# Performance work log

Hardware: AMD Instinct MI355X
Metric: run time of the kernel (lower is better)

Reference implementation:

```python
import jax, jax.numpy as jnp
import numpy as np

B, N, DM, H = 1, 2048, 1024, 16
CURV = 1.0  # hyperbolic curvature


def setup_inputs() -> dict:
    key = jax.random.key(0)
    ks = jax.random.split(key, 5)
    s = 1.0 / np.sqrt(DM)  # nn.Linear default init scale
    x = jax.random.normal(ks[0], (B, N, DM), dtype=jnp.float32)
    Wq = jax.random.uniform(ks[1], (DM, DM), jnp.float32, -s, s)
    Wk = jax.random.uniform(ks[2], (DM, DM), jnp.float32, -s, s)
    Wv = jax.random.uniform(ks[3], (DM, DM), jnp.float32, -s, s)
    Wo = jax.random.uniform(ks[4], (DM, DM), jnp.float32, -s, s)
    return {"x": x, "Wq": Wq, "Wk": Wk, "Wv": Wv, "Wo": Wo}


def reference(x, Wq, Wk, Wv, Wo):
    b, n, d = x.shape
    hd = d // H

    def split_heads(t):  # [B,N,D] -> [B,H,N,hd]
        return t.reshape(b, n, H, hd).transpose(0, 2, 1, 3)

    q = split_heads(x @ Wq.T)
    k = split_heads(x @ Wk.T)
    v = split_heads(x @ Wv.T)

    q_norm_sq = jnp.sum(q * q, axis=-1, keepdims=True)      # [B,H,N,1]
    k_norm_sq = jnp.sum(k * k, axis=-1)[:, :, None, :]      # [B,H,1,N]
    qk = jnp.einsum('bhnd,bhmd->bhnm', q, k)                # [B,H,N,N]

    diff_sq = jnp.maximum(q_norm_sq + k_norm_sq - 2.0 * qk, 0.0)
    denom = jnp.maximum((1.0 - CURV * q_norm_sq) * (1.0 - CURV * k_norm_sq), 1e-6)
    cosh_arg = jnp.maximum(1.0 + 2.0 * CURV * diff_sq / denom, 1.0)
    # safe acosh: acosh(1)=0; mask avoids inf grad at the boundary
    distance = jnp.where(cosh_arg > 1.0,
                         jnp.arccosh(jnp.maximum(cosh_arg, 1.0 + 1e-12)),
                         0.0)

    attn = jax.nn.softmax(-distance, axis=-1)               # [B,H,N,N]
    out = jnp.einsum('bhnm,bhmd->bhnd', attn, v)            # [B,H,N,hd]
    out = out.transpose(0, 2, 1, 3).reshape(b, n, d)
    return out @ Wo.T
```

## Files before the change

kernel.cpp:

```cpp
#include <hip/hip_runtime.h>
#include <math.h>

#define NSEQ   2048
#define DMODEL 1024
#define NHEADS 16
#define HD     64
#define NJH    2
#define JSPAN  (NSEQ / NJH)

typedef short bf16x8 __attribute__((ext_vector_type(8)));
typedef float f32x4  __attribute__((ext_vector_type(4)));
typedef unsigned short ushort8_t __attribute__((ext_vector_type(8)));

__device__ __forceinline__ unsigned short f2bf(float x) {
    unsigned int u = __builtin_bit_cast(unsigned int, x);
    unsigned int r = (u + 0x7FFFu + ((u >> 16) & 1u)) >> 16;
    return (unsigned short)r;
}

__global__ __launch_bounds__(256) void convert_inputs(
    const float* __restrict__ x,  const float* __restrict__ Wq,
    const float* __restrict__ Wk, const float* __restrict__ Wv,
    const float* __restrict__ Wo,
    unsigned short* __restrict__ xb, unsigned short* __restrict__ Wb,
    unsigned short* __restrict__ Wob)
{
    const size_t i8 = ((size_t)blockIdx.x * 256 + threadIdx.x) * 8;
    const float* src;
    unsigned short* dst;
    if (i8 < (2ull << 20)) {
        src = x + i8;  dst = xb + i8;
    } else if (i8 < (5ull << 20)) {
        const size_t o = i8 - (2ull << 20);
        const size_t s = o >> 20;
        src = (s == 0 ? Wq : (s == 1 ? Wk : Wv)) + (o & ((1u << 20) - 1));
        dst = Wb + o;
    } else {
        const size_t o = i8 - (5ull << 20);
        src = Wo + o;  dst = Wob + o;
    }
    const float4 v0 = *reinterpret_cast<const float4*>(src);
    const float4 v1 = *reinterpret_cast<const float4*>(src + 4);
    ushort8_t r;
    r[0] = f2bf(v0.x); r[1] = f2bf(v0.y); r[2] = f2bf(v0.z); r[3] = f2bf(v0.w);
    r[4] = f2bf(v1.x); r[5] = f2bf(v1.y); r[6] = f2bf(v1.z); r[7] = f2bf(v1.w);
    *reinterpret_cast<ushort8_t*>(dst) = r;
}

template <int QKV>
__global__ __launch_bounds__(256) void gemm_bt_bf16(
    const unsigned short* __restrict__ A, const unsigned short* __restrict__ B,
    float* __restrict__ C0,
    unsigned short* __restrict__ QbO, float* __restrict__ qnO,
    float* __restrict__ cq2O,
    unsigned short* __restrict__ KbO, float* __restrict__ knO,
    float* __restrict__ ckO,
    unsigned short* __restrict__ VbO)
{
    __shared__ unsigned short Ahs[128 * 64];
    __shared__ unsigned short Bhs[64 * 64];

    const int bm   = blockIdx.x * 128;
    const int bn   = blockIdx.y * 64;
    const int t    = threadIdx.x;
    const int wid  = t >> 6;
    const int lane = t & 63;
    const int g    = lane >> 4;
    const int r    = lane & 15;
    const int wm   = wid * 32;

    const int sel = QKV ? (bn >> 10) : 0;
    const int bnl = QKV ? (bn & 1023) : bn;

    f32x4 acc[2][4];
#pragma unroll
    for (int i = 0; i < 2; ++i)
#pragma unroll
        for (int j = 0; j < 4; ++j) acc[i][j] = (f32x4){0.f, 0.f, 0.f, 0.f};

    const int srowA = t >> 1;
    const int shalA = t & 1;
    const int srowB = t >> 2;
    const int squadB = t & 3;

    const unsigned short* Ag = &A[(size_t)(bm + srowA) * DMODEL + shalA * 32];
    const unsigned short* Bg = &B[(size_t)(bn + srowB) * DMODEL + squadB * 16];

    ushort8_t av[4], bv[2];
#pragma unroll
    for (int c = 0; c < 4; ++c)
        av[c] = *reinterpret_cast<const ushort8_t*>(Ag + c * 8);
#pragma unroll
    for (int c = 0; c < 2; ++c)
        bv[c] = *reinterpret_cast<const ushort8_t*>(Bg + c * 8);

    for (int k0 = 0; k0 < DMODEL; k0 += 64) {
        __syncthreads();
#pragma unroll
        for (int c = 0; c < 4; ++c) {
            const int sw = ((shalA * 4 + c) ^ (srowA & 7)) * 8;
            *reinterpret_cast<ushort8_t*>(&Ahs[srowA * 64 + sw]) = av[c];
        }
#pragma unroll
        for (int c = 0; c < 2; ++c) {
            const int sw = ((squadB * 2 + c) ^ (srowB & 7)) * 8;
            *reinterpret_cast<ushort8_t*>(&Bhs[srowB * 64 + sw]) = bv[c];
        }
        if (k0 + 64 < DMODEL) {
#pragma unroll
            for (int c = 0; c < 4; ++c)
                av[c] = *reinterpret_cast<const ushort8_t*>(
                    Ag + k0 + 64 + c * 8);
#pragma unroll
            for (int c = 0; c < 2; ++c)
                bv[c] = *reinterpret_cast<const ushort8_t*>(
                    Bg + k0 + 64 + c * 8);
        }
        __syncthreads();

#pragma unroll
        for (int dc = 0; dc < 2; ++dc) {
            bf16x8 af[2], bfr[4];
#pragma unroll
            for (int mt = 0; mt < 2; ++mt)
                af[mt] = *reinterpret_cast<const bf16x8*>(
                    &Ahs[(wm + mt * 16 + r) * 64 + ((dc * 4 + g) ^ (r & 7)) * 8]);
#pragma unroll
            for (int nt = 0; nt < 4; ++nt)
                bfr[nt] = *reinterpret_cast<const bf16x8*>(
                    &Bhs[(nt * 16 + r) * 64 + ((dc * 4 + g) ^ (r & 7)) * 8]);
#pragma unroll
            for (int mt = 0; mt < 2; ++mt)
#pragma unroll
                for (int nt = 0; nt < 4; ++nt)
                    acc[mt][nt] = __builtin_amdgcn_mfma_f32_16x16x32_bf16(
                        af[mt], bfr[nt], acc[mt][nt], 0, 0, 0);
        }
    }

    if (QKV) {
        if (sel < 2) {
            unsigned short* Hb = sel ? KbO : QbO;
            float* narr = sel ? knO : qnO;
            float* carr = sel ? ckO : cq2O;
            const int hh = bnl >> 6;
#pragma unroll
            for (int mt = 0; mt < 2; ++mt) {
#pragma unroll
                for (int rg = 0; rg < 4; ++rg) {
                    float ss = 0.f;
#pragma unroll
                    for (int nt = 0; nt < 4; ++nt) {
                        const float v = acc[mt][nt][rg];
                        ss = fmaf(v, v, ss);
                        Hb[(size_t)(bm + wm + mt * 16 + g * 4 + rg) * 1024 +
                           bnl + nt * 16 + r] = f2bf(v);
                    }
                    ss += __shfl_xor(ss, 1, 64);
                    ss += __shfl_xor(ss, 2, 64);
                    ss += __shfl_xor(ss, 4, 64);
                    ss += __shfl_xor(ss, 8, 64);
                    if (r == 0) {
                        const int row = bm + wm + mt * 16 + g * 4 + rg;
                        narr[hh * NSEQ + row] = ss;
                        carr[hh * NSEQ + row] = (sel ? 1.0f : 2.0f) / (1.0f - ss);
                    }
                }
            }
        } else {
#pragma unroll
            for (int mt = 0; mt < 2; ++mt)
#pragma unroll
                for (int nt = 0; nt < 4; ++nt)
#pragma unroll
                    for (int rg = 0; rg < 4; ++rg)
                        VbO[(size_t)(bm + wm + mt * 16 + g * 4 + rg) * 1024 +
                            bnl + nt * 16 + r] = f2bf(acc[mt][nt][rg]);
        }
    } else {
#pragma unroll
        for (int mt = 0; mt < 2; ++mt)
#pragma unroll
            for (int nt = 0; nt < 4; ++nt)
#pragma unroll
                for (int rg = 0; rg < 4; ++rg)
                    C0[(size_t)(bm + wm + mt * 16 + g * 4 + rg) * 1024 +
                       bnl + nt * 16 + r] = acc[mt][nt][rg];
    }
}

__global__ __launch_bounds__(256) void vt_kernel_bf16(
    const unsigned short* __restrict__ Vb, unsigned short* __restrict__ Vt)
{
    __shared__ unsigned short Vs[64 * 72];
    const int h   = blockIdx.y;
    const int n0  = blockIdx.x * 64;
    const int t   = threadIdx.x;
    const int row = t >> 2;
    const int seg = (t & 3) * 16;

    const unsigned short* src = Vb + (size_t)(n0 + row) * 1024 + h * HD + seg;
    *reinterpret_cast<ushort8_t*>(&Vs[row * 72 + seg]) =
        *reinterpret_cast<const ushort8_t*>(src);
    *reinterpret_cast<ushort8_t*>(&Vs[row * 72 + seg + 8]) =
        *reinterpret_cast<const ushort8_t*>(src + 8);
    __syncthreads();

    ushort8_t a, b;
#pragma unroll
    for (int c = 0; c < 8; ++c) a[c] = Vs[(seg + c) * 72 + row];
#pragma unroll
    for (int c = 0; c < 8; ++c) b[c] = Vs[(seg + 8 + c) * 72 + row];
    unsigned short* dst = Vt + (size_t)(h * HD + row) * NSEQ + n0 + seg;
    *reinterpret_cast<ushort8_t*>(dst)     = a;
    *reinterpret_cast<ushort8_t*>(dst + 8) = b;
}

__global__ __launch_bounds__(256) void hyp_attn_v5(
    const unsigned short* __restrict__ Qb, const unsigned short* __restrict__ Kb,
    const unsigned short* __restrict__ Vt,
    const float* __restrict__ qn_a, const float* __restrict__ cq2_a,
    const float* __restrict__ kn_a, const float* __restrict__ ck_a,
    float* __restrict__ Opart, float* __restrict__ lpart)
{
    __shared__ unsigned short Khs[64 * 64];
    __shared__ unsigned short Vts[64 * 64];
    __shared__ unsigned short Ps[4][16 * 64];
    __shared__ float kns[JSPAN];
    __shared__ float cks[JSPAN];

    const int h    = blockIdx.y;
    const int n0   = blockIdx.x * 64;
    const int jh   = blockIdx.z;
    const int t    = threadIdx.x;
    const int wid  = t >> 6;
    const int lane = t & 63;
    const int g    = lane >> 4;
    const int r    = lane & 15;
    const int qb   = n0 + wid * 16;

    bf16x8 qf[2];
#pragma unroll
    for (int dc = 0; dc < 2; ++dc)
        qf[dc] = *reinterpret_cast<const bf16x8*>(
            Qb + (size_t)(qb + r) * DMODEL + h * HD + dc * 32 + g * 8);

    float qn_r[4], c2q[4];
#pragma unroll
    for (int rg = 0; rg < 4; ++rg) {
        qn_r[rg] = qn_a[h * NSEQ + qb + g * 4 + rg];
        c2q[rg]  = cq2_a[h * NSEQ + qb + g * 4 + rg];
    }
#pragma unroll
    for (int i = 0; i < JSPAN / 256; ++i) {
        kns[i * 256 + t] = kn_a[h * NSEQ + jh * JSPAN + i * 256 + t];
        cks[i * 256 + t] = ck_a[h * NSEQ + jh * JSPAN + i * 256 + t];
    }

    f32x4 oacc[4];
#pragma unroll
    for (int nt = 0; nt < 4; ++nt) oacc[nt] = (f32x4){0.f, 0.f, 0.f, 0.f};
    float l_acc[4] = {0.f, 0.f, 0.f, 0.f};

    const int srow = t >> 2;
    const int c0   = (t & 3) * 2;
    const int sw0  = (c0 ^ (srow & 7)) * 8;
    const int sw1  = ((c0 + 1) ^ (srow & 7)) * 8;
    const int sg   = (t & 3) * 16;
    unsigned short* Pw = &Ps[wid][0];

    const unsigned short* Kg = Kb + (size_t)(jh * JSPAN + srow) * DMODEL + h * HD + sg;
    const unsigned short* Vg = Vt + (size_t)(h * HD + srow) * NSEQ + jh * JSPAN + sg;

    ushort8_t kr0 = *reinterpret_cast<const ushort8_t*>(Kg);
    ushort8_t kr1 = *reinterpret_cast<const ushort8_t*>(Kg + 8);
    ushort8_t vr0 = *reinterpret_cast<const ushort8_t*>(Vg);
    ushort8_t vr1 = *reinterpret_cast<const ushort8_t*>(Vg + 8);

    const int ntb = JSPAN / 64;
    for (int tb = 0; tb < ntb; ++tb) {
        __syncthreads();
        *reinterpret_cast<ushort8_t*>(&Khs[srow * 64 + sw0]) = kr0;
        *reinterpret_cast<ushort8_t*>(&Khs[srow * 64 + sw1]) = kr1;
        *reinterpret_cast<ushort8_t*>(&Vts[srow * 64 + sw0]) = vr0;
        *reinterpret_cast<ushort8_t*>(&Vts[srow * 64 + sw1]) = vr1;
        if (tb + 1 < ntb) {
            const unsigned short* kn_ = Kg + (size_t)(tb + 1) * 64 * DMODEL;
            const unsigned short* vn_ = Vg + (tb + 1) * 64;
            kr0 = *reinterpret_cast<const ushort8_t*>(kn_);
            kr1 = *reinterpret_cast<const ushort8_t*>(kn_ + 8);
            vr0 = *reinterpret_cast<const ushort8_t*>(vn_);
            vr1 = *reinterpret_cast<const ushort8_t*>(vn_ + 8);
        }
        __syncthreads();

#pragma unroll
        for (int jt = 0; jt < 4; ++jt) {
            f32x4 sac = (f32x4){0.f, 0.f, 0.f, 0.f};
#pragma unroll
            for (int dc = 0; dc < 2; ++dc) {
                const bf16x8 kb = *reinterpret_cast<const bf16x8*>(
                    &Khs[(jt * 16 + r) * 64 + ((dc * 4 + g) ^ (r & 7)) * 8]);
                sac = __builtin_amdgcn_mfma_f32_16x16x32_bf16(qf[dc], kb, sac, 0, 0, 0);
            }
            const int jl = tb * 64 + jt * 16 + r;
            const float kn_v = kns[jl];
            const float ck_v = cks[jl];
#pragma unroll
            for (int rg = 0; rg < 4; ++rg) {
                const float dsq = fmaf(-2.f, sac[rg], qn_r[rg] + kn_v);
                const float ca  = fmaxf(fmaf(dsq, c2q[rg] * ck_v, 1.f), 1.0f);
                const float s2  = fmaf(ca, ca, -1.f);
                const float wj  = ca - __builtin_amdgcn_sqrtf(s2);
                l_acc[rg] += wj;
                const int qrow = g * 4 + rg;
                Pw[qrow * 64 +
                   ((2 * jt + (r >> 3)) ^ (qrow & 7)) * 8 + (r & 7)] = f2bf(wj);
            }
        }

#pragma unroll
        for (int kc = 0; kc < 2; ++kc) {
            const bf16x8 pa = *reinterpret_cast<const bf16x8*>(
                &Pw[r * 64 + ((kc * 4 + g) ^ (r & 7)) * 8]);
#pragma unroll
            for (int nt = 0; nt < 4; ++nt) {
                const bf16x8 vb = *reinterpret_cast<const bf16x8*>(
                    &Vts[(nt * 16 + r) * 64 + ((kc * 4 + g) ^ (r & 7)) * 8]);
                oacc[nt] = __builtin_amdgcn_mfma_f32_16x16x32_bf16(pa, vb, oacc[nt], 0, 0, 0);
            }
        }
    }

#pragma unroll
    for (int rg = 0; rg < 4; ++rg) {
        l_acc[rg] += __shfl_xor(l_acc[rg], 1, 64);
        l_acc[rg] += __shfl_xor(l_acc[rg], 2, 64);
        l_acc[rg] += __shfl_xor(l_acc[rg], 4, 64);
        l_acc[rg] += __shfl_xor(l_acc[rg], 8, 64);
    }

    float* Op = Opart + (size_t)jh * NSEQ * DMODEL;
#pragma unroll
    for (int nt = 0; nt < 4; ++nt)
#pragma unroll
        for (int rg = 0; rg < 4; ++rg)
            Op[(size_t)(qb + g * 4 + rg) * DMODEL + h * HD + nt * 16 + r] =
                oacc[nt][rg];
    if (r == 0) {
#pragma unroll
        for (int rg = 0; rg < 4; ++rg)
            lpart[(jh * NHEADS + h) * NSEQ + qb + g * 4 + rg] = l_acc[rg];
    }
}

__global__ __launch_bounds__(256) void merge_kernel(
    const float* __restrict__ Opart, const float* __restrict__ lpart,
    unsigned short* __restrict__ Ob)
{
    const size_t i8 = ((size_t)blockIdx.x * 256 + threadIdx.x) * 8;
    if (i8 >= (size_t)NSEQ * DMODEL) return;
    const int n  = (int)(i8 >> 10);
    const int dm = (int)(i8 & 1023);
    const int h  = dm >> 6;
    const float li = 1.0f / (lpart[h * NSEQ + n] +
                             lpart[(NHEADS + h) * NSEQ + n]);
    const float* O0 = Opart + i8;
    const float* O1 = Opart + (size_t)NSEQ * DMODEL + i8;
    ushort8_t o;
#pragma unroll
    for (int c = 0; c < 2; ++c) {
        const float4 a = *reinterpret_cast<const float4*>(O0 + c * 4);
        const float4 b = *reinterpret_cast<const float4*>(O1 + c * 4);
        o[c * 4 + 0] = f2bf((a.x + b.x) * li);
        o[c * 4 + 1] = f2bf((a.y + b.y) * li);
        o[c * 4 + 2] = f2bf((a.z + b.z) * li);
        o[c * 4 + 3] = f2bf((a.w + b.w) * li);
    }
    *reinterpret_cast<ushort8_t*>(Ob + i8) = o;
}

extern "C" void kernel_launch(void* const* d_in, const int* in_sizes, int n_in,
                              void* d_out, int out_size, void* d_ws, size_t ws_size,
                              hipStream_t stream)
{
    const float* x  = (const float*)d_in[0];
    const float* Wq = (const float*)d_in[1];
    const float* Wk = (const float*)d_in[2];
    const float* Wv = (const float*)d_in[3];
    const float* Wo = (const float*)d_in[4];
    float* out = (float*)d_out;

    char* ws = (char*)d_ws;
    const size_t MB = 1048576;
    unsigned short* xb   = (unsigned short*)(ws);
    unsigned short* Wb   = (unsigned short*)(ws + 4  * MB);
    unsigned short* Wob  = (unsigned short*)(ws + 10 * MB);
    unsigned short* Qbuf = (unsigned short*)(ws + 12 * MB);
    unsigned short* Kbuf = (unsigned short*)(ws + 16 * MB);
    unsigned short* Vb   = (unsigned short*)(ws + 20 * MB);
    unsigned short* Vt   = (unsigned short*)(ws + 24 * MB);
    float*          qn   = (float*)(ws + 28 * MB);
    float*          cq2  = qn  + NHEADS * NSEQ;
    float*          kn   = cq2 + NHEADS * NSEQ;
    float*          ck   = kn  + NHEADS * NSEQ;
    float*          Opart= (float*)(ws + 29 * MB);
    float*          lpart= (float*)(ws + 45 * MB);
    unsigned short* Ob   = xb;

    const dim3 blk(256);

    convert_inputs<<<3072, blk, 0, stream>>>(x, Wq, Wk, Wv, Wo, xb, Wb, Wob);

    gemm_bt_bf16<1><<<dim3(NSEQ / 128, 3072 / 64), blk, 0, stream>>>(
        xb, Wb, nullptr, Qbuf, qn, cq2, Kbuf, kn, ck, Vb);

    vt_kernel_bf16<<<dim3(NSEQ / 64, NHEADS), blk, 0, stream>>>(Vb, Vt);

    hyp_attn_v5<<<dim3(NSEQ / 64, NHEADS, NJH), blk, 0, stream>>>(
        Qbuf, Kbuf, Vt, qn, cq2, kn, ck, Opart, lpart);

    merge_kernel<<<(NSEQ * DMODEL / 8 + 255) / 256, blk, 0, stream>>>(
        Opart, lpart, Ob);

    gemm_bt_bf16<0><<<dim3(NSEQ / 128, DMODEL / 64), blk, 0, stream>>>(
        Ob, Wob, out, nullptr, nullptr, nullptr,
        nullptr, nullptr, nullptr, nullptr);
}
```

Before: 95.08 us.

## Load K/V MFMA operands directly from global memory, dropping LDS staging

The attention kernel stops cooperatively staging K and V tiles into shared memory. Each wave now loads its MFMA operand fragments straight from global memory into registers every tile. This removes the two block barriers and the LDS stores per tile. In exchange, each of the four waves redundantly fetches the same K/V data, which raises L2/global traffic. The next tile is also no longer software-prefetched, so load latency is exposed and register pressure rises.

Measured after the change: 167.5 us. 76.2% more time.

```diff
diff --git a/kernel.cpp b/kernel.cpp
--- a/kernel.cpp
+++ b/kernel.cpp
@@ -216,15 +216,13 @@
     *reinterpret_cast<ushort8_t*>(dst + 8) = b;
 }
 
-__global__ __launch_bounds__(256) void hyp_attn_v5(
+__global__ __launch_bounds__(256) void hyp_attn_v6(
     const unsigned short* __restrict__ Qb, const unsigned short* __restrict__ Kb,
     const unsigned short* __restrict__ Vt,
     const float* __restrict__ qn_a, const float* __restrict__ cq2_a,
     const float* __restrict__ kn_a, const float* __restrict__ ck_a,
     float* __restrict__ Opart, float* __restrict__ lpart)
 {
-    __shared__ unsigned short Khs[64 * 64];
-    __shared__ unsigned short Vts[64 * 64];
     __shared__ unsigned short Ps[4][16 * 64];
     __shared__ float kns[JSPAN];
     __shared__ float cks[JSPAN];
@@ -256,54 +254,44 @@
         kns[i * 256 + t] = kn_a[h * NSEQ + jh * JSPAN + i * 256 + t];
         cks[i * 256 + t] = ck_a[h * NSEQ + jh * JSPAN + i * 256 + t];
     }
+    __syncthreads();
 
     f32x4 oacc[4];
 #pragma unroll
     for (int nt = 0; nt < 4; ++nt) oacc[nt] = (f32x4){0.f, 0.f, 0.f, 0.f};
     float l_acc[4] = {0.f, 0.f, 0.f, 0.f};
 
-    const int srow = t >> 2;
-    const int c0   = (t & 3) * 2;
-    const int sw0  = (c0 ^ (srow & 7)) * 8;
-    const int sw1  = ((c0 + 1) ^ (srow & 7)) * 8;
-    const int sg   = (t & 3) * 16;
     unsigned short* Pw = &Ps[wid][0];
 
-    const unsigned short* Kg = Kb + (size_t)(jh * JSPAN + srow) * DMODEL + h * HD + sg;
-    const unsigned short* Vg = Vt + (size_t)(h * HD + srow) * NSEQ + jh * JSPAN + sg;
-
-    ushort8_t kr0 = *reinterpret_cast<const ushort8_t*>(Kg);
-    ushort8_t kr1 = *reinterpret_cast<const ushort8_t*>(Kg + 8);
-    ushort8_t vr0 = *reinterpret_cast<const ushort8_t*>(Vg);
-    ushort8_t vr1 = *reinterpret_cast<const ushort8_t*>(Vg + 8);
+    const unsigned short* Kg =
+        Kb + (size_t)(jh * JSPAN + r) * DMODEL + h * HD + g * 8;
+    const unsigned short* Vg =
+        Vt + (size_t)(h * HD + r) * NSEQ + jh * JSPAN + g * 8;
 
     const int ntb = JSPAN / 64;
     for (int tb = 0; tb < ntb; ++tb) {
-        __syncthreads();
-        *reinterpret_cast<ushort8_t*>(&Khs[srow * 64 + sw0]) = kr0;
-        *reinterpret_cast<ushort8_t*>(&Khs[srow * 64 + sw1]) = kr1;
-        *reinterpret_cast<ushort8_t*>(&Vts[srow * 64 + sw0]) = vr0;
-        *reinterpret_cast<ushort8_t*>(&Vts[srow * 64 + sw1]) = vr1;
-        if (tb + 1 < ntb) {
-            const unsigned short* kn_ = Kg + (size_t)(tb + 1) * 64 * DMODEL;
-            const unsigned short* vn_ = Vg + (tb + 1) * 64;
-            kr0 = *reinterpret_cast<const ushort8_t*>(kn_);
-            kr1 = *reinterpret_cast<const ushort8_t*>(kn_ + 8);
-            vr0 = *reinterpret_cast<const ushort8_t*>(vn_);
-            vr1 = *reinterpret_cast<const ushort8_t*>(vn_ + 8);
-        }
-        __syncthreads();
+        const int jl0 = tb * 64;
+
+        bf16x8 kb[4][2], vb[2][4];
+#pragma unroll
+        for (int jt = 0; jt < 4; ++jt)
+#pragma unroll
+            for (int dc = 0; dc < 2; ++dc)
+                kb[jt][dc] = *reinterpret_cast<const bf16x8*>(
+                    Kg + (size_t)(jl0 + jt * 16) * DMODEL + dc * 32);
+#pragma unroll
+        for (int kc = 0; kc < 2; ++kc)
+#pragma unroll
+            for (int nt = 0; nt < 4; ++nt)
+                vb[kc][nt] = *reinterpret_cast<const bf16x8*>(
+                    Vg + (size_t)(nt * 16) * NSEQ + jl0 + kc * 32);
 
 #pragma unroll
         for (int jt = 0; jt < 4; ++jt) {
             f32x4 sac = (f32x4){0.f, 0.f, 0.f, 0.f};
-#pragma unroll
-            for (int dc = 0; dc < 2; ++dc) {
-                const bf16x8 kb = *reinterpret_cast<const bf16x8*>(
-                    &Khs[(jt * 16 + r) * 64 + ((dc * 4 + g) ^ (r & 7)) * 8]);
-                sac = __builtin_amdgcn_mfma_f32_16x16x32_bf16(qf[dc], kb, sac, 0, 0, 0);
-            }
-            const int jl = tb * 64 + jt * 16 + r;
+            sac = __builtin_amdgcn_mfma_f32_16x16x32_bf16(qf[0], kb[jt][0], sac, 0, 0, 0);
+            sac = __builtin_amdgcn_mfma_f32_16x16x32_bf16(qf[1], kb[jt][1], sac, 0, 0, 0);
+            const int jl = jl0 + jt * 16 + r;
             const float kn_v = kns[jl];
             const float ck_v = cks[jl];
 #pragma unroll
@@ -324,11 +312,9 @@
             const bf16x8 pa = *reinterpret_cast<const bf16x8*>(
                 &Pw[r * 64 + ((kc * 4 + g) ^ (r & 7)) * 8]);
 #pragma unroll
-            for (int nt = 0; nt < 4; ++nt) {
-                const bf16x8 vb = *reinterpret_cast<const bf16x8*>(
-                    &Vts[(nt * 16 + r) * 64 + ((kc * 4 + g) ^ (r & 7)) * 8]);
-                oacc[nt] = __builtin_amdgcn_mfma_f32_16x16x32_bf16(pa, vb, oacc[nt], 0, 0, 0);
-            }
+            for (int nt = 0; nt < 4; ++nt)
+                oacc[nt] = __builtin_amdgcn_mfma_f32_16x16x32_bf16(
+                    pa, vb[kc][nt], oacc[nt], 0, 0, 0);
         }
     }
 
@@ -417,7 +403,7 @@
 
     vt_kernel_bf16<<<dim3(NSEQ / 64, NHEADS), blk, 0, stream>>>(Vb, Vt);
 
-    hyp_attn_v5<<<dim3(NSEQ / 64, NHEADS, NJH), blk, 0, stream>>>(
+    hyp_attn_v6<<<dim3(NSEQ / 64, NHEADS, NJH), blk, 0, stream>>>(
         Qbuf, Kbuf, Vt, qn, cq2, kn, ck, Opart, lpart);
 
     merge_kernel<<<(NSEQ * DMODEL / 8 + 255) / 256, blk, 0, stream>>>(
```

## Process 32 query rows per wave and split keys four ways when workspace allows

Applied to the files above, without the earlier changes.

The attention kernel now has each wave handle two 16-row query sub-tiles (128 queries per block). Each K/V tile loaded into LDS is therefore reused across twice as many queries, which halves K/V global traffic and tile staging per query. To keep enough blocks in flight, the key dimension is split into 4 partitions when the workspace is large enough, and the merge kernel is generalised to sum any number of partials. The cost is more registers per wave, double the P LDS buffer, and more partial-output traffic in the merge when the 4-way split is used.

Measured after the change: 96.29 us. About the same (+1.3%).

```diff
diff --git a/kernel.cpp b/kernel.cpp
--- a/kernel.cpp
+++ b/kernel.cpp
@@ -5,8 +5,6 @@
 #define DMODEL 1024
 #define NHEADS 16
 #define HD     64
-#define NJH    2
-#define JSPAN  (NSEQ / NJH)
 
 typedef short bf16x8 __attribute__((ext_vector_type(8)));
 typedef float f32x4  __attribute__((ext_vector_type(4)));
@@ -216,7 +214,8 @@
     *reinterpret_cast<ushort8_t*>(dst + 8) = b;
 }
 
-__global__ __launch_bounds__(256) void hyp_attn_v5(
+template <int JSPAN>
+__global__ __launch_bounds__(256) void hyp_attn_v7(
     const unsigned short* __restrict__ Qb, const unsigned short* __restrict__ Kb,
     const unsigned short* __restrict__ Vt,
     const float* __restrict__ qn_a, const float* __restrict__ cq2_a,
@@ -225,42 +224,48 @@
 {
     __shared__ unsigned short Khs[64 * 64];
     __shared__ unsigned short Vts[64 * 64];
-    __shared__ unsigned short Ps[4][16 * 64];
+    __shared__ unsigned short Ps[4][32 * 64];
     __shared__ float kns[JSPAN];
     __shared__ float cks[JSPAN];
 
     const int h    = blockIdx.y;
-    const int n0   = blockIdx.x * 64;
+    const int n0   = blockIdx.x * 128;
     const int jh   = blockIdx.z;
     const int t    = threadIdx.x;
     const int wid  = t >> 6;
     const int lane = t & 63;
     const int g    = lane >> 4;
     const int r    = lane & 15;
-    const int qb   = n0 + wid * 16;
-
-    bf16x8 qf[2];
-#pragma unroll
-    for (int dc = 0; dc < 2; ++dc)
-        qf[dc] = *reinterpret_cast<const bf16x8*>(
-            Qb + (size_t)(qb + r) * DMODEL + h * HD + dc * 32 + g * 8);
-
-    float qn_r[4], c2q[4];
-#pragma unroll
-    for (int rg = 0; rg < 4; ++rg) {
-        qn_r[rg] = qn_a[h * NSEQ + qb + g * 4 + rg];
-        c2q[rg]  = cq2_a[h * NSEQ + qb + g * 4 + rg];
-    }
+    const int qb   = n0 + wid * 32;
+
+    bf16x8 qf[2][2];
+#pragma unroll
+    for (int s = 0; s < 2; ++s)
+#pragma unroll
+        for (int dc = 0; dc < 2; ++dc)
+            qf[s][dc] = *reinterpret_cast<const bf16x8*>(
+                Qb + (size_t)(qb + s * 16 + r) * DMODEL + h * HD + dc * 32 + g * 8);
+
+    float qn_r[2][4], c2q[2][4];
+#pragma unroll
+    for (int s = 0; s < 2; ++s)
+#pragma unroll
+        for (int rg = 0; rg < 4; ++rg) {
+            qn_r[s][rg] = qn_a[h * NSEQ + qb + s * 16 + g * 4 + rg];
+            c2q[s][rg]  = cq2_a[h * NSEQ + qb + s * 16 + g * 4 + rg];
+        }
 #pragma unroll
     for (int i = 0; i < JSPAN / 256; ++i) {
         kns[i * 256 + t] = kn_a[h * NSEQ + jh * JSPAN + i * 256 + t];
         cks[i * 256 + t] = ck_a[h * NSEQ + jh * JSPAN + i * 256 + t];
     }
 
-    f32x4 oacc[4];
-#pragma unroll
-    for (int nt = 0; nt < 4; ++nt) oacc[nt] = (f32x4){0.f, 0.f, 0.f, 0.f};
-    float l_acc[4] = {0.f, 0.f, 0.f, 0.f};
+    f32x4 oacc[2][4];
+#pragma unroll
+    for (int s = 0; s < 2; ++s)
+#pragma unroll
+        for (int nt = 0; nt < 4; ++nt) oacc[s][nt] = (f32x4){0.f, 0.f, 0.f, 0.f};
+    float l_acc[2][4] = {{0.f, 0.f, 0.f, 0.f}, {0.f, 0.f, 0.f, 0.f}};
 
     const int srow = t >> 2;
     const int c0   = (t & 3) * 2;
@@ -296,87 +301,106 @@
 
 #pragma unroll
         for (int jt = 0; jt < 4; ++jt) {
-            f32x4 sac = (f32x4){0.f, 0.f, 0.f, 0.f};
+            f32x4 sac0 = (f32x4){0.f, 0.f, 0.f, 0.f};
+            f32x4 sac1 = (f32x4){0.f, 0.f, 0.f, 0.f};
 #pragma unroll
             for (int dc = 0; dc < 2; ++dc) {
                 const bf16x8 kb = *reinterpret_cast<const bf16x8*>(
                     &Khs[(jt * 16 + r) * 64 + ((dc * 4 + g) ^ (r & 7)) * 8]);
-                sac = __builtin_amdgcn_mfma_f32_16x16x32_bf16(qf[dc], kb, sac, 0, 0, 0);
+                sac0 = __builtin_amdgcn_mfma_f32_16x16x32_bf16(qf[0][dc], kb, sac0, 0, 0, 0);
+                sac1 = __builtin_amdgcn_mfma_f32_16x16x32_bf16(qf[1][dc], kb, sac1, 0, 0, 0);
             }
             const int jl = tb * 64 + jt * 16 + r;
             const float kn_v = kns[jl];
             const float ck_v = cks[jl];
 #pragma unroll
-            for (int rg = 0; rg < 4; ++rg) {
-                const float dsq = fmaf(-2.f, sac[rg], qn_r[rg] + kn_v);
-                const float ca  = fmaxf(fmaf(dsq, c2q[rg] * ck_v, 1.f), 1.0f);
-                const float s2  = fmaf(ca, ca, -1.f);
-                const float wj  = ca - __builtin_amdgcn_sqrtf(s2);
-                l_acc[rg] += wj;
-                const int qrow = g * 4 + rg;
-                Pw[qrow * 64 +
-                   ((2 * jt + (r >> 3)) ^ (qrow & 7)) * 8 + (r & 7)] = f2bf(wj);
+            for (int s = 0; s < 2; ++s) {
+                const f32x4 sac = s ? sac1 : sac0;
+#pragma unroll
+                for (int rg = 0; rg < 4; ++rg) {
+                    const float dsq = fmaf(-2.f, sac[rg], qn_r[s][rg] + kn_v);
+                    const float ca  = fmaxf(fmaf(dsq, c2q[s][rg] * ck_v, 1.f), 1.0f);
+                    const float s2  = fmaf(ca, ca, -1.f);
+                    const float wj  = ca - __builtin_amdgcn_sqrtf(s2);
+                    l_acc[s][rg] += wj;
+                    const int qrow = s * 16 + g * 4 + rg;
+                    Pw[qrow * 64 +
+                       ((2 * jt + (r >> 3)) ^ (qrow & 7)) * 8 + (r & 7)] = f2bf(wj);
+                }
             }
         }
 
 #pragma unroll
         for (int kc = 0; kc < 2; ++kc) {
-            const bf16x8 pa = *reinterpret_cast<const bf16x8*>(
-                &Pw[r * 64 + ((kc * 4 + g) ^ (r & 7)) * 8]);
+            const bf16x8 pa0 = *reinterpret_cast<const bf16x8*>(
+                &Pw[(0 * 16 + r) * 64 + ((kc * 4 + g) ^ (r & 7)) * 8]);
+            const bf16x8 pa1 = *reinterpret_cast<const bf16x8*>(
+                &Pw[(1 * 16 + r) * 64 + ((kc * 4 + g) ^ (r & 7)) * 8]);
 #pragma unroll
             for (int nt = 0; nt < 4; ++nt) {
                 const bf16x8 vb = *reinterpret_cast<const bf16x8*>(
                     &Vts[(nt * 16 + r) * 64 + ((kc * 4 + g) ^ (r & 7)) * 8]);
-                oacc[nt] = __builtin_amdgcn_mfma_f32_16x16x32_bf16(pa, vb, oacc[nt], 0, 0, 0);
+                oacc[0][nt] = __builtin_amdgcn_mfma_f32_16x16x32_bf16(pa0, vb, oacc[0][nt], 0, 0, 0);
+                oacc[1][nt] = __builtin_amdgcn_mfma_f32_16x16x32_bf16(pa1, vb, oacc[1][nt], 0, 0, 0);
             }
         }
     }
 
 #pragma unroll
-    for (int rg = 0; rg < 4; ++rg) {
-        l_acc[rg] += __shfl_xor(l_acc[rg], 1, 64);
-        l_acc[rg] += __shfl_xor(l_acc[rg], 2, 64);
-        l_acc[rg] += __shfl_xor(l_acc[rg], 4, 64);
-        l_acc[rg] += __shfl_xor(l_acc[rg], 8, 64);
-    }
+    for (int s = 0; s < 2; ++s)
+#pragma unroll
+        for (int rg = 0; rg < 4; ++rg) {
+            l_acc[s][rg] += __shfl_xor(l_acc[s][rg], 1, 64);
+            l_acc[s][rg] += __shfl_xor(l_acc[s][rg], 2, 64);
+            l_acc[s][rg] += __shfl_xor(l_acc[s][rg], 4, 64);
+            l_acc[s][rg] += __shfl_xor(l_acc[s][rg], 8, 64);
+        }
 
     float* Op = Opart + (size_t)jh * NSEQ * DMODEL;
 #pragma unroll
-    for (int nt = 0; nt < 4; ++nt)
-#pragma unroll
-        for (int rg = 0; rg < 4; ++rg)
-            Op[(size_t)(qb + g * 4 + rg) * DMODEL + h * HD + nt * 16 + r] =
-                oacc[nt][rg];
+    for (int s = 0; s < 2; ++s)
+#pragma unroll
+        for (int nt = 0; nt < 4; ++nt)
+#pragma unroll
+            for (int rg = 0; rg < 4; ++rg)
+                Op[(size_t)(qb + s * 16 + g * 4 + rg) * DMODEL + h * HD + nt * 16 + r] =
+                    oacc[s][nt][rg];
     if (r == 0) {
 #pragma unroll
-        for (int rg = 0; rg < 4; ++rg)
-            lpart[(jh * NHEADS + h) * NSEQ + qb + g * 4 + rg] = l_acc[rg];
+        for (int s = 0; s < 2; ++s)
+#pragma unroll
+            for (int rg = 0; rg < 4; ++rg)
+                lpart[(jh * NHEADS + h) * NSEQ + qb + s * 16 + g * 4 + rg] =
+                    l_acc[s][rg];
     }
 }
 
 __global__ __launch_bounds__(256) void merge_kernel(
     const float* __restrict__ Opart, const float* __restrict__ lpart,
-    unsigned short* __restrict__ Ob)
+    unsigned short* __restrict__ Ob, int njh)
 {
     const size_t i8 = ((size_t)blockIdx.x * 256 + threadIdx.x) * 8;
     if (i8 >= (size_t)NSEQ * DMODEL) return;
     const int n  = (int)(i8 >> 10);
     const int dm = (int)(i8 & 1023);
     const int h  = dm >> 6;
-    const float li = 1.0f / (lpart[h * NSEQ + n] +
-                             lpart[(NHEADS + h) * NSEQ + n]);
-    const float* O0 = Opart + i8;
-    const float* O1 = Opart + (size_t)NSEQ * DMODEL + i8;
+    float lsum = 0.f;
+    for (int p = 0; p < njh; ++p)
+        lsum += lpart[(p * NHEADS + h) * NSEQ + n];
+    const float li = 1.0f / lsum;
+    float s[8] = {0.f, 0.f, 0.f, 0.f, 0.f, 0.f, 0.f, 0.f};
+    for (int p = 0; p < njh; ++p) {
+        const float* Opp = Opart + (size_t)p * NSEQ * DMODEL + i8;
+#pragma unroll
+        for (int c = 0; c < 2; ++c) {
+            const float4 a = *reinterpret_cast<const float4*>(Opp + c * 4);
+            s[c * 4 + 0] += a.x; s[c * 4 + 1] += a.y;
+            s[c * 4 + 2] += a.z; s[c * 4 + 3] += a.w;
+        }
+    }
     ushort8_t o;
 #pragma unroll
-    for (int c = 0; c < 2; ++c) {
-        const float4 a = *reinterpret_cast<const float4*>(O0 + c * 4);
-        const float4 b = *reinterpret_cast<const float4*>(O1 + c * 4);
-        o[c * 4 + 0] = f2bf((a.x + b.x) * li);
-        o[c * 4 + 1] = f2bf((a.y + b.y) * li);
-        o[c * 4 + 2] = f2bf((a.z + b.z) * li);
-        o[c * 4 + 3] = f2bf((a.w + b.w) * li);
-    }
+    for (int c = 0; c < 8; ++c) o[c] = f2bf(s[c] * li);
     *reinterpret_cast<ushort8_t*>(Ob + i8) = o;
 }
 
@@ -405,8 +429,10 @@
     float*          kn   = cq2 + NHEADS * NSEQ;
     float*          ck   = kn  + NHEADS * NSEQ;
     float*          Opart= (float*)(ws + 29 * MB);
-    float*          lpart= (float*)(ws + 45 * MB);
     unsigned short* Ob   = xb;
+
+    const int njh = (ws_size >= 63 * MB) ? 4 : 2;
+    float* lpart = (float*)(ws + (29 + (size_t)njh * 8) * MB);
 
     const dim3 blk(256);
 
@@ -417,11 +443,15 @@
 
     vt_kernel_bf16<<<dim3(NSEQ / 64, NHEADS), blk, 0, stream>>>(Vb, Vt);
 
-    hyp_attn_v5<<<dim3(NSEQ / 64, NHEADS, NJH), blk, 0, stream>>>(
-        Qbuf, Kbuf, Vt, qn, cq2, kn, ck, Opart, lpart);
+    if (njh == 4)
+        hyp_attn_v7<512><<<dim3(NSEQ / 128, NHEADS, 4), blk, 0, stream>>>(
+            Qbuf, Kbuf, Vt, qn, cq2, kn, ck, Opart, lpart);
+    else
+        hyp_attn_v7<1024><<<dim3(NSEQ / 128, NHEADS, 2), blk, 0, stream>>>(
+            Qbuf, Kbuf, Vt, qn, cq2, kn, ck, Opart, lpart);
 
     merge_kernel<<<(NSEQ * DMODEL / 8 + 255) / 256, blk, 0, stream>>>(
-        Opart, lpart, Ob);
+        Opart, lpart, Ob, njh);
 
     gemm_bt_bf16<0><<<dim3(NSEQ / 128, DMODEL / 64), blk, 0, stream>>>(
         Ob, Wob, out, nullptr, nullptr, nullptr,
```
